# Kernel optimization log

Measured on AMD Instinct MI355X. Metric: run time of the kernel, lower is better.

Reference implementation:

```python
import jax, jax.numpy as jnp
import numpy as np

B, S, DX, DH = 8, 4096, 512, 512


def log_g(x):
    # log of g(x) where g(x) = relu(x)+0.5 for x>=0 and sigmoid-like for x<0
    return jnp.where(x >= 0, jnp.log(jax.nn.relu(x) + 0.5), -jax.nn.softplus(-x))


def parallel_scan(log_coeffs, log_values):
    # log_coeffs: (B, S, H); log_values: (B, S+1, H)
    # Heinsen log-space linear-recurrence scan.
    a_star = jnp.pad(jnp.cumsum(log_coeffs, axis=1), ((0, 0), (1, 0), (0, 0)))  # (B,S+1,H)
    log_h = a_star + jax.lax.cumlogsumexp(log_values - a_star, axis=1)
    return log_h[:, 1:]  # (B, S, H)


def setup_inputs() -> dict:
    key = jax.random.key(0)
    ks = jax.random.split(key, 8)
    sx = 1.0 / np.sqrt(DX)
    sh = 1.0 / np.sqrt(DH)
    return {
        "x": jax.random.normal(ks[0], (B, S, DX), dtype=jnp.float32),
        "h_prev": jax.random.uniform(ks[1], (B, 1, DH), dtype=jnp.float32),
        "Wz": jax.random.uniform(ks[2], (DX, DH), jnp.float32, -sx, sx),
        "bz": jax.random.uniform(ks[3], (DH,), jnp.float32, -sx, sx),
        "Wh": jax.random.uniform(ks[4], (DX, DH), jnp.float32, -sx, sx),
        "bh": jax.random.uniform(ks[5], (DH,), jnp.float32, -sx, sx),
        "Wo": jax.random.uniform(ks[6], (DH, DX), jnp.float32, -sh, sh),
        "bo": jax.random.uniform(ks[7], (DX,), jnp.float32, -sh, sh),
    }


def reference(x, h_prev, Wz, bz, Wh, bh, Wo, bo):
    k = jnp.einsum('bsd,dh->bsh', x, Wz) + bz           # gate pre-activation
    tilde_h = jnp.einsum('bsd,dh->bsh', x, Wh) + bh     # candidate hidden
    log_z = -jax.nn.softplus(-k)
    log_one_minus_z = -jax.nn.softplus(k)
    log_h_prev = log_g(h_prev)                          # (B,1,H)
    log_tilde_h = log_g(tilde_h)                        # (B,S,H)
    log_vals = jnp.concatenate([log_h_prev, log_z + log_tilde_h], axis=1)  # (B,S+1,H)
    log_h = parallel_scan(log_one_minus_z, log_vals)    # (B,S,H)
    h = jnp.exp(log_h)
    out = jnp.einsum('bsh,hd->bsd', h, Wo) + bo         # (B,S,DX)
    return out
```

## Files before the change

### kernel.cpp

```cpp
#include <hip/hip_runtime.h>


using bf16x8 = __attribute__((ext_vector_type(8))) short;
using f32x4  = __attribute__((ext_vector_type(4))) float;

#define NB 8
#define NS 4096
#define ND 512
#define SC 64
#define WU 32
#define NCHUNK (NS/SC)

__device__ __forceinline__ unsigned short f2bf(float f) {
  unsigned u = __float_as_uint(f);
  u += 0x7fffu + ((u >> 16) & 1u);
  return (unsigned short)(u >> 16);
}

__device__ __forceinline__ void gload16(const void* g, void* l) {
  __builtin_amdgcn_global_load_lds(
      (const __attribute__((address_space(1))) void*)g,
      (__attribute__((address_space(3))) void*)l, 16, 0, 0);
}

__global__ void prep_kernel(const float4* __restrict__ x4, ushort4* __restrict__ xb4, int n4,
                            const float* __restrict__ Wz, const float* __restrict__ Wh,
                            const float* __restrict__ Wo,
                            unsigned short* __restrict__ WzhT, unsigned short* __restrict__ WoT) {
  const int stride = gridDim.x * blockDim.x;
  const int t0 = blockIdx.x * blockDim.x + threadIdx.x;
  for (int i = t0; i < n4; i += stride) {
    float4 f = x4[i];
    ushort4 o;
    o.x = f2bf(f.x); o.y = f2bf(f.y); o.z = f2bf(f.z); o.w = f2bf(f.w);
    xb4[i] = o;
  }
  for (int i = t0; i < 1024 * 512; i += stride) {
    int n = i >> 9, kk = i & 511;
    int g32 = n >> 5, w = n & 31;
    int h = g32 * 16 + (w & 15);
    float val = (w < 16) ? Wz[kk * 512 + h] : Wh[kk * 512 + h];
    WzhT[i] = f2bf(val);
  }
  for (int j = t0; j < 512 * 512; j += stride) {
    int d = j >> 9, hh = j & 511;
    WoT[j] = f2bf(Wo[hh * 512 + d]);
  }
}

__device__ __forceinline__ void stage_tile(const unsigned short* __restrict__ A,
                                           const unsigned short* __restrict__ Bt,
                                           int m0, int n0, int kt, int tid,
                                           unsigned short* As, unsigned short* Bs) {
  int row = tid >> 2, c16 = tid & 3;
  int srcb = (c16 * 16) ^ (((row >> 1) & 3) << 4);
  gload16(A  + (size_t)(m0 + row) * 512 + kt + (srcb >> 1),
          As + tid * 8);
  gload16(Bt + (size_t)(n0 + row) * 512 + kt + (srcb >> 1),
          Bs + tid * 8);
}

__device__ __forceinline__ void compute_tile(const unsigned short* As, const unsigned short* Bs,
                                             int lane, int wm, int wn, f32x4 (&acc)[4][2]) {
  bf16x8 af[4], bfr[2];
  const int kq = (lane >> 4) << 4;
#pragma unroll
  for (int m = 0; m < 4; ++m) {
    int row = wm * 64 + m * 16 + (lane & 15);
    af[m] = *(const bf16x8*)((const char*)As + row * 64 + (kq ^ (((row >> 1) & 3) << 4)));
  }
#pragma unroll
  for (int n = 0; n < 2; ++n) {
    int row = wn * 32 + n * 16 + (lane & 15);
    bfr[n] = *(const bf16x8*)((const char*)Bs + row * 64 + (kq ^ (((row >> 1) & 3) << 4)));
  }
#pragma unroll
  for (int m = 0; m < 4; ++m)
#pragma unroll
    for (int n = 0; n < 2; ++n)
      acc[m][n] = __builtin_amdgcn_mfma_f32_16x16x32_bf16(af[m], bfr[n], acc[m][n], 0, 0, 0);
}

__device__ __forceinline__ void gemm_core(const unsigned short* __restrict__ A,
                                          const unsigned short* __restrict__ Bt,
                                          int m0, int n0,
                                          unsigned short (&As)[2][128 * 32],
                                          unsigned short (&Bs)[2][128 * 32],
                                          f32x4 (&acc)[4][2]) {
  const int tid  = threadIdx.x;
  const int lane = tid & 63;
  const int wave = tid >> 6;
  const int wm = wave & 1, wn = wave >> 1;

  const f32x4 zero = {0.f, 0.f, 0.f, 0.f};
#pragma unroll
  for (int m = 0; m < 4; ++m)
#pragma unroll
    for (int n = 0; n < 2; ++n) acc[m][n] = zero;

  stage_tile(A, Bt, m0, n0, 0, tid, As[0], Bs[0]);
  __syncthreads();
#pragma unroll
  for (int t = 0; t < 15; ++t) {
    const int cur = t & 1;
    stage_tile(A, Bt, m0, n0, (t + 1) * 32, tid, As[cur ^ 1], Bs[cur ^ 1]);
    compute_tile(As[cur], Bs[cur], lane, wm, wn, acc);
    __syncthreads();
  }
  compute_tile(As[1], Bs[1], lane, wm, wn, acc);
}

__global__ __launch_bounds__(512, 8) void gemm1_kernel(const unsigned short* __restrict__ xb,
                                                       const unsigned short* __restrict__ WzhT,
                                                       const float* __restrict__ bz,
                                                       const float* __restrict__ bh,
                                                       unsigned int* __restrict__ cv) {
  __shared__ unsigned short As[2][128 * 32];
  __shared__ unsigned short Bs[2][128 * 32];
  int bid = blockIdx.x;
  int x = bid & 7, i = bid >> 3;
  int nt = i & 7;
  int mt = x + ((i >> 3) << 3);
  int m0 = mt * 128, n0 = nt * 128;
  f32x4 acc[4][2];
  gemm_core(xb, WzhT, m0, n0, As, Bs, acc);

  const int lane = threadIdx.x & 63;
  const int wave = threadIdx.x >> 6;
  const int wm = wave & 1, wn = wave >> 1;
  int h = ((n0 + wn * 32) >> 1) + (lane & 15);
  float bzv = bz[h], bhv = bh[h];
#pragma unroll
  for (int m = 0; m < 4; ++m) {
#pragma unroll
    for (int r = 0; r < 4; ++r) {
      int rowg = m0 + wm * 64 + m * 16 + ((lane >> 4) << 2) + r;
      float kv = acc[m][0][r] + bzv;
      float tv = acc[m][1][r] + bhv;
      float z  = 1.f / (1.f + __expf(-kv));
      float c  = 1.f / (1.f + __expf(kv));
      float gg = (tv >= 0.f) ? (tv + 0.5f) : (1.f / (1.f + __expf(-tv)));
      float vv = z * gg;
      cv[(size_t)rowg * 512 + h] = ((unsigned)f2bf(vv) << 16) | (unsigned)f2bf(c);
    }
  }
}

__global__ __launch_bounds__(512) void scan_kernel(const unsigned int* __restrict__ cv,
                                                   const float* __restrict__ hprev,
                                                   unsigned short* __restrict__ hbuf) {
  int b = blockIdx.x >> 6;
  int chunk = blockIdx.x & 63;
  int h = threadIdx.x;
  int s0 = chunk * SC;
  float acc;
  int sstart;
  if (chunk == 0) {
    float hp = hprev[b * 512 + h];
    acc = (hp >= 0.f) ? (hp + 0.5f) : (1.f / (1.f + __expf(-hp)));
    sstart = 0;
  } else {
    acc = 0.f;
    sstart = s0 - WU;
  }
  const unsigned int* p = cv + ((size_t)(b * NS + sstart) << 9) + h;
  for (int s = sstart; s < s0; s += 8) {
    unsigned int u[8];
#pragma unroll
    for (int j = 0; j < 8; ++j) u[j] = p[(size_t)j << 9];
    p += (size_t)8 << 9;
#pragma unroll
    for (int j = 0; j < 8; ++j)
      acc = fmaf(__uint_as_float(u[j] << 16), acc, __uint_as_float(u[j] & 0xffff0000u));
  }
  unsigned short* q = hbuf + ((size_t)(b * NS + s0) << 9) + h;
  for (int s = 0; s < SC; s += 8) {
    unsigned int u[8];
#pragma unroll
    for (int j = 0; j < 8; ++j) u[j] = p[(size_t)j << 9];
    p += (size_t)8 << 9;
#pragma unroll
    for (int j = 0; j < 8; ++j) {
      acc = fmaf(__uint_as_float(u[j] << 16), acc, __uint_as_float(u[j] & 0xffff0000u));
      q[(size_t)j << 9] = f2bf(acc);
    }
    q += (size_t)8 << 9;
  }
}

__global__ __launch_bounds__(512, 8) void gemm2_kernel(const unsigned short* __restrict__ hb,
                                                       const unsigned short* __restrict__ WoT,
                                                       const float* __restrict__ bo,
                                                       float* __restrict__ out) {
  __shared__ unsigned short As[2][128 * 32];
  __shared__ unsigned short Bs[2][128 * 32];
  int bid = blockIdx.x;
  int x = bid & 7, i = bid >> 3;
  int nt = i & 3;
  int mt = x + ((i >> 2) << 3);
  int m0 = mt * 128, n0 = nt * 128;
  f32x4 acc[4][2];
  gemm_core(hb, WoT, m0, n0, As, Bs, acc);

  const int lane = threadIdx.x & 63;
  const int wave = threadIdx.x >> 6;
  const int wm = wave & 1, wn = wave >> 1;
#pragma unroll
  for (int n = 0; n < 2; ++n) {
    int colg = n0 + wn * 32 + n * 16 + (lane & 15);
    float bov = bo[colg];
#pragma unroll
    for (int m = 0; m < 4; ++m) {
#pragma unroll
      for (int r = 0; r < 4; ++r) {
        int rowg = m0 + wm * 64 + m * 16 + ((lane >> 4) << 2) + r;
        out[(size_t)rowg * 512 + colg] = acc[m][n][r] + bov;
      }
    }
  }
}

extern "C" void kernel_launch(void* const* d_in, const int* in_sizes, int n_in,
                              void* d_out, int out_size, void* d_ws, size_t ws_size,
                              hipStream_t stream) {
  const float* x     = (const float*)d_in[0];
  const float* hprev = (const float*)d_in[1];
  const float* Wz    = (const float*)d_in[2];
  const float* bz    = (const float*)d_in[3];
  const float* Wh    = (const float*)d_in[4];
  const float* bh    = (const float*)d_in[5];
  const float* Wo    = (const float*)d_in[6];
  const float* bo    = (const float*)d_in[7];
  float* out = (float*)d_out;

  char* ws = (char*)d_ws;
  unsigned short* xb   = (unsigned short*)(ws);
  unsigned short* hbuf = (unsigned short*)(ws);
  unsigned short* WzhT = (unsigned short*)(ws + ((size_t)32 << 20));
  unsigned short* WoT  = (unsigned short*)(ws + ((size_t)33 << 20));
  unsigned int* cv = (unsigned int*)d_out;

  prep_kernel<<<2048, 256, 0, stream>>>((const float4*)x, (ushort4*)xb, (NB * NS * ND) / 4,
                                        Wz, Wh, Wo, WzhT, WoT);
  gemm1_kernel<<<2048, 512, 0, stream>>>(xb, WzhT, bz, bh, cv);
  scan_kernel<<<NB * NCHUNK, 512, 0, stream>>>(cv, hprev, hbuf);
  gemm2_kernel<<<1024, 512, 0, stream>>>(hbuf, WoT, bo, out);
}
```

Before: 242.9 us.

## Use 256x256 GEMM tiles with BK=64 and phased barrier-scheduled pipelining

Both GEMMs move from 128x128 tiles with BK=32 to 256x256 tiles with BK=64. The main loop becomes an explicitly phased schedule: global-to-LDS loads are issued in halves and interleaved with MFMA quadrants, separated by s_barrier, s_setprio and vmcnt waits. The aim is to raise arithmetic intensity per LDS byte, reuse each fragment more, and overlap memory with compute. In exchange the grid shrinks to 512 and 256 blocks, occupancy drops to 2 blocks per CU with large register use, and the hand-written waitcnt logic risks races or tail imbalance.

```diff
diff --git a/kernel.cpp b/kernel.cpp
--- a/kernel.cpp
+++ b/kernel.cpp
@@ -48,100 +48,174 @@
   }
 }
 
-__device__ __forceinline__ void stage_tile(const unsigned short* __restrict__ A,
-                                           const unsigned short* __restrict__ Bt,
-                                           int m0, int n0, int kt, int tid,
-                                           unsigned short* As, unsigned short* Bs) {
-  int row = tid >> 2, c16 = tid & 3;
-  int srcb = (c16 * 16) ^ (((row >> 1) & 3) << 4);
-  gload16(A  + (size_t)(m0 + row) * 512 + kt + (srcb >> 1),
-          As + tid * 8);
-  gload16(Bt + (size_t)(n0 + row) * 512 + kt + (srcb >> 1),
-          Bs + tid * 8);
-}
-
-__device__ __forceinline__ void compute_tile(const unsigned short* As, const unsigned short* Bs,
-                                             int lane, int wm, int wn, f32x4 (&acc)[4][2]) {
-  bf16x8 af[4], bfr[2];
+__device__ __forceinline__ void stageH(const unsigned short* __restrict__ G, int row0,
+                                       int kt, int half, unsigned short* L, int tid) {
+#pragma unroll
+  for (int it = 0; it < 2; ++it) {
+    int flat = it * 512 + tid;
+    int row = half * 128 + (flat >> 3);
+    int c16 = flat & 7;
+    int srcb = (c16 * 16) ^ ((row & 7) << 4);
+    gload16(G + (size_t)(row0 + row) * 512 + kt + (srcb >> 1),
+            L + half * 8192 + flat * 8);
+  }
+}
+
+__device__ __forceinline__ void readA(const unsigned short* As, int wm, int mh, int lane,
+                                      bf16x8 (&af)[4][2]) {
+  const int r0 = wm * 128 + mh * 64 + (lane & 15);
   const int kq = (lane >> 4) << 4;
 #pragma unroll
   for (int m = 0; m < 4; ++m) {
-    int row = wm * 64 + m * 16 + (lane & 15);
-    af[m] = *(const bf16x8*)((const char*)As + row * 64 + (kq ^ (((row >> 1) & 3) << 4)));
-  }
+    const int row = r0 + m * 16;
+    const int sw = (row & 7) << 4;
+#pragma unroll
+    for (int ks = 0; ks < 2; ++ks)
+      af[m][ks] = *(const bf16x8*)((const char*)As + row * 128 + ((ks * 64 + kq) ^ sw));
+  }
+}
+
+__device__ __forceinline__ void readB(const unsigned short* Bs, int wn, int nh, int lane,
+                                      bf16x8 (&bf)[2][2]) {
+  const int r0 = wn * 64 + nh * 32 + (lane & 15);
+  const int kq = (lane >> 4) << 4;
 #pragma unroll
   for (int n = 0; n < 2; ++n) {
-    int row = wn * 32 + n * 16 + (lane & 15);
-    bfr[n] = *(const bf16x8*)((const char*)Bs + row * 64 + (kq ^ (((row >> 1) & 3) << 4)));
-  }
-#pragma unroll
-  for (int m = 0; m < 4; ++m)
-#pragma unroll
-    for (int n = 0; n < 2; ++n)
-      acc[m][n] = __builtin_amdgcn_mfma_f32_16x16x32_bf16(af[m], bfr[n], acc[m][n], 0, 0, 0);
-}
-
-__device__ __forceinline__ void gemm_core(const unsigned short* __restrict__ A,
-                                          const unsigned short* __restrict__ Bt,
-                                          int m0, int n0,
-                                          unsigned short (&As)[2][128 * 32],
-                                          unsigned short (&Bs)[2][128 * 32],
-                                          f32x4 (&acc)[4][2]) {
+    const int row = r0 + n * 16;
+    const int sw = (row & 7) << 4;
+#pragma unroll
+    for (int ks = 0; ks < 2; ++ks)
+      bf[n][ks] = *(const bf16x8*)((const char*)Bs + row * 128 + ((ks * 64 + kq) ^ sw));
+  }
+}
+
+__device__ __forceinline__ void mfmaQ(int MH, int NH, const bf16x8 (&af)[4][2],
+                                      const bf16x8 (&bf)[2][2], f32x4 (&acc)[8][4]) {
+#pragma unroll
+  for (int ks = 0; ks < 2; ++ks)
+#pragma unroll
+    for (int m = 0; m < 4; ++m)
+#pragma unroll
+      for (int n = 0; n < 2; ++n)
+        acc[MH * 4 + m][NH * 2 + n] =
+            __builtin_amdgcn_mfma_f32_16x16x32_bf16(af[m][ks], bf[n][ks],
+                                                    acc[MH * 4 + m][NH * 2 + n], 0, 0, 0);
+}
+
+#define PH_PRE  do { asm volatile("s_barrier" ::: "memory");                 \
+                     asm volatile("s_waitcnt lgkmcnt(0)" ::: "memory");      \
+                     __builtin_amdgcn_sched_barrier(0);                      \
+                     __builtin_amdgcn_s_setprio(1); } while (0)
+#define PH_POST do { __builtin_amdgcn_s_setprio(0);                          \
+                     asm volatile("s_barrier" ::: "memory"); } while (0)
+#define PH_POST_G4 do { __builtin_amdgcn_s_setprio(0);                       \
+                     asm volatile("s_waitcnt vmcnt(4)" ::: "memory");        \
+                     asm volatile("s_barrier" ::: "memory"); } while (0)
+#define PH_POST_G0 do { __builtin_amdgcn_s_setprio(0);                       \
+                     asm volatile("s_waitcnt vmcnt(0)" ::: "memory");        \
+                     asm volatile("s_barrier" ::: "memory"); } while (0)
+
+template <bool LAST>
+__device__ __forceinline__ void iter8(const unsigned short* __restrict__ Ag,
+                                      const unsigned short* __restrict__ Bg,
+                                      int m0, int n0, int kt0,
+                                      unsigned short (&As)[2][16384],
+                                      unsigned short (&Bs)[2][16384],
+                                      int tid, int lane, int wm, int wn,
+                                      f32x4 (&acc)[8][4]) {
+  bf16x8 af[4][2], b0[2][2], b1[2][2];
+  const int kt1 = kt0 + 64, kt2 = kt0 + 128, kt3 = kt0 + 192;
+  readA(As[0], wm, 0, lane, af);
+  readB(Bs[0], wn, 0, lane, b0);
+  stageH(Ag, m0, kt1, 0, As[1], tid);
+  PH_PRE; mfmaQ(0, 0, af, b0, acc); PH_POST;
+  readB(Bs[0], wn, 1, lane, b1);
+  stageH(Ag, m0, kt1, 1, As[1], tid);
+  PH_PRE; mfmaQ(0, 1, af, b1, acc); PH_POST;
+  readA(As[0], wm, 1, lane, af);
+  if (!LAST) stageH(Bg, n0, kt2, 0, Bs[0], tid);
+  PH_PRE; mfmaQ(1, 0, af, b0, acc); PH_POST;
+  if (!LAST) stageH(Bg, n0, kt2, 1, Bs[0], tid);
+  PH_PRE; mfmaQ(1, 1, af, b1, acc);
+  if (LAST) { PH_POST_G0; } else { PH_POST_G4; }
+  readA(As[1], wm, 0, lane, af);
+  readB(Bs[1], wn, 0, lane, b0);
+  if (!LAST) stageH(Ag, m0, kt2, 0, As[0], tid);
+  PH_PRE; mfmaQ(0, 0, af, b0, acc); PH_POST;
+  readB(Bs[1], wn, 1, lane, b1);
+  if (!LAST) stageH(Ag, m0, kt2, 1, As[0], tid);
+  PH_PRE; mfmaQ(0, 1, af, b1, acc); PH_POST;
+  readA(As[1], wm, 1, lane, af);
+  if (!LAST) stageH(Bg, n0, kt3, 0, Bs[1], tid);
+  PH_PRE; mfmaQ(1, 0, af, b0, acc); PH_POST;
+  if (!LAST) stageH(Bg, n0, kt3, 1, Bs[1], tid);
+  PH_PRE; mfmaQ(1, 1, af, b1, acc);
+  if (LAST) { __builtin_amdgcn_s_setprio(0); } else { PH_POST_G4; }
+}
+
+__device__ __forceinline__ void gemm_core256(const unsigned short* __restrict__ Ag,
+                                             const unsigned short* __restrict__ Bg,
+                                             int m0, int n0,
+                                             unsigned short (&As)[2][16384],
+                                             unsigned short (&Bs)[2][16384],
+                                             f32x4 (&acc)[8][4]) {
   const int tid  = threadIdx.x;
   const int lane = tid & 63;
   const int wave = tid >> 6;
-  const int wm = wave & 1, wn = wave >> 1;
+  const int wm = wave >> 2, wn = wave & 3;
 
   const f32x4 zero = {0.f, 0.f, 0.f, 0.f};
 #pragma unroll
-  for (int m = 0; m < 4; ++m)
-#pragma unroll
-    for (int n = 0; n < 2; ++n) acc[m][n] = zero;
-
-  stage_tile(A, Bt, m0, n0, 0, tid, As[0], Bs[0]);
-  __syncthreads();
-#pragma unroll
-  for (int t = 0; t < 15; ++t) {
-    const int cur = t & 1;
-    stage_tile(A, Bt, m0, n0, (t + 1) * 32, tid, As[cur ^ 1], Bs[cur ^ 1]);
-    compute_tile(As[cur], Bs[cur], lane, wm, wn, acc);
-    __syncthreads();
-  }
-  compute_tile(As[1], Bs[1], lane, wm, wn, acc);
-}
-
-__global__ __launch_bounds__(512, 8) void gemm1_kernel(const unsigned short* __restrict__ xb,
+  for (int a = 0; a < 8; ++a)
+#pragma unroll
+    for (int b = 0; b < 4; ++b) acc[a][b] = zero;
+
+  stageH(Ag, m0, 0, 0, As[0], tid);  stageH(Ag, m0, 0, 1, As[0], tid);
+  stageH(Bg, n0, 0, 0, Bs[0], tid);  stageH(Bg, n0, 0, 1, Bs[0], tid);
+  stageH(Bg, n0, 64, 0, Bs[1], tid); stageH(Bg, n0, 64, 1, Bs[1], tid);
+  asm volatile("s_waitcnt vmcnt(4)" ::: "memory");
+  asm volatile("s_barrier" ::: "memory");
+
+  for (int i = 0; i < 3; ++i)
+    iter8<false>(Ag, Bg, m0, n0, i * 128, As, Bs, tid, lane, wm, wn, acc);
+  iter8<true>(Ag, Bg, m0, n0, 384, As, Bs, tid, lane, wm, wn, acc);
+}
+
+__global__ __launch_bounds__(512, 2) void gemm1_kernel(const unsigned short* __restrict__ xb,
                                                        const unsigned short* __restrict__ WzhT,
                                                        const float* __restrict__ bz,
                                                        const float* __restrict__ bh,
                                                        unsigned int* __restrict__ cv) {
-  __shared__ unsigned short As[2][128 * 32];
-  __shared__ unsigned short Bs[2][128 * 32];
+  __shared__ unsigned short As[2][16384];
+  __shared__ unsigned short Bs[2][16384];
   int bid = blockIdx.x;
   int x = bid & 7, i = bid >> 3;
-  int nt = i & 7;
-  int mt = x + ((i >> 3) << 3);
-  int m0 = mt * 128, n0 = nt * 128;
-  f32x4 acc[4][2];
-  gemm_core(xb, WzhT, m0, n0, As, Bs, acc);
+  int nt = i & 3;
+  int mt = x + ((i >> 2) << 3);
+  int m0 = mt * 256, n0 = nt * 256;
+  f32x4 acc[8][4];
+  gemm_core256(xb, WzhT, m0, n0, As, Bs, acc);
 
   const int lane = threadIdx.x & 63;
   const int wave = threadIdx.x >> 6;
-  const int wm = wave & 1, wn = wave >> 1;
-  int h = ((n0 + wn * 32) >> 1) + (lane & 15);
-  float bzv = bz[h], bhv = bh[h];
-#pragma unroll
-  for (int m = 0; m < 4; ++m) {
-#pragma unroll
-    for (int r = 0; r < 4; ++r) {
-      int rowg = m0 + wm * 64 + m * 16 + ((lane >> 4) << 2) + r;
-      float kv = acc[m][0][r] + bzv;
-      float tv = acc[m][1][r] + bhv;
-      float z  = 1.f / (1.f + __expf(-kv));
-      float c  = 1.f / (1.f + __expf(kv));
-      float gg = (tv >= 0.f) ? (tv + 0.5f) : (1.f / (1.f + __expf(-tv)));
-      float vv = z * gg;
-      cv[(size_t)rowg * 512 + h] = ((unsigned)f2bf(vv) << 16) | (unsigned)f2bf(c);
+  const int wm = wave >> 2, wn = wave & 3;
+#pragma unroll
+  for (int nh = 0; nh < 2; ++nh) {
+    int h = ((n0 + wn * 64 + nh * 32) >> 1) + (lane & 15);
+    float bzv = bz[h], bhv = bh[h];
+#pragma unroll
+    for (int a = 0; a < 8; ++a) {
+#pragma unroll
+      for (int r = 0; r < 4; ++r) {
+        int rowg = m0 + wm * 128 + (a >> 2) * 64 + (a & 3) * 16 + ((lane >> 4) << 2) + r;
+        float kv = acc[a][nh * 2][r]     + bzv;
+        float tv = acc[a][nh * 2 + 1][r] + bhv;
+        float z  = 1.f / (1.f + __expf(-kv));
+        float c  = 1.f / (1.f + __expf(kv));
+        float gg = (tv >= 0.f) ? (tv + 0.5f) : (1.f / (1.f + __expf(-tv)));
+        float vv = z * gg;
+        cv[(size_t)rowg * 512 + h] = ((unsigned)f2bf(vv) << 16) | (unsigned)f2bf(c);
+      }
     }
   }
 }
@@ -188,33 +262,36 @@
   }
 }
 
-__global__ __launch_bounds__(512, 8) void gemm2_kernel(const unsigned short* __restrict__ hb,
+__global__ __launch_bounds__(512, 2) void gemm2_kernel(const unsigned short* __restrict__ hb,
                                                        const unsigned short* __restrict__ WoT,
                                                        const float* __restrict__ bo,
                                                        float* __restrict__ out) {
-  __shared__ unsigned short As[2][128 * 32];
-  __shared__ unsigned short Bs[2][128 * 32];
+  __shared__ unsigned short As[2][16384];
+  __shared__ unsigned short Bs[2][16384];
   int bid = blockIdx.x;
   int x = bid & 7, i = bid >> 3;
-  int nt = i & 3;
-  int mt = x + ((i >> 2) << 3);
-  int m0 = mt * 128, n0 = nt * 128;
-  f32x4 acc[4][2];
-  gemm_core(hb, WoT, m0, n0, As, Bs, acc);
+  int nt = i & 1;
+  int mt = x + ((i >> 1) << 3);
+  int m0 = mt * 256, n0 = nt * 256;
+  f32x4 acc[8][4];
+  gemm_core256(hb, WoT, m0, n0, As, Bs, acc);
 
   const int lane = threadIdx.x & 63;
   const int wave = threadIdx.x >> 6;
-  const int wm = wave & 1, wn = wave >> 1;
-#pragma unroll
-  for (int n = 0; n < 2; ++n) {
-    int colg = n0 + wn * 32 + n * 16 + (lane & 15);
-    float bov = bo[colg];
-#pragma unroll
-    for (int m = 0; m < 4; ++m) {
-#pragma unroll
-      for (int r = 0; r < 4; ++r) {
-        int rowg = m0 + wm * 64 + m * 16 + ((lane >> 4) << 2) + r;
-        out[(size_t)rowg * 512 + colg] = acc[m][n][r] + bov;
+  const int wm = wave >> 2, wn = wave & 3;
+#pragma unroll
+  for (int nh = 0; nh < 2; ++nh) {
+#pragma unroll
+    for (int n = 0; n < 2; ++n) {
+      int colg = n0 + wn * 64 + nh * 32 + n * 16 + (lane & 15);
+      float bov = bo[colg];
+#pragma unroll
+      for (int a = 0; a < 8; ++a) {
+#pragma unroll
+        for (int r = 0; r < 4; ++r) {
+          int rowg = m0 + wm * 128 + (a >> 2) * 64 + (a & 3) * 16 + ((lane >> 4) << 2) + r;
+          out[(size_t)rowg * 512 + colg] = acc[a][nh * 2 + n][r] + bov;
+        }
       }
     }
   }
@@ -242,7 +319,7 @@
 
   prep_kernel<<<2048, 256, 0, stream>>>((const float4*)x, (ushort4*)xb, (NB * NS * ND) / 4,
                                         Wz, Wh, Wo, WzhT, WoT);
-  gemm1_kernel<<<2048, 512, 0, stream>>>(xb, WzhT, bz, bh, cv);
+  gemm1_kernel<<<512, 512, 0, stream>>>(xb, WzhT, bz, bh, cv);
   scan_kernel<<<NB * NCHUNK, 512, 0, stream>>>(cv, hprev, hbuf);
-  gemm2_kernel<<<1024, 512, 0, stream>>>(hbuf, WoT, bo, out);
-}
+  gemm2_kernel<<<256, 512, 0, stream>>>(hbuf, WoT, bo, out);
+}
```

After: 232.1 us. 1.05x faster.
